# Performance work log

Measured on AMD Instinct MI355X. Metric: run time of the kernel, lower is better.

Reference implementation:

```python
import jax, jax.numpy as jnp
import numpy as np

OUT_RANGE = 6.0
OUT_SHIFT = -3.0


def setup_inputs() -> dict:
    key = jax.random.key(0)
    ks = jax.random.split(key, 6)
    B, T = 128, 64
    A, V, X = 48, 48, 96
    PF = 128
    fdim = (A + 1) * (V + 1) * (X + 1)  # 232897
    return {
        "audio_h": jax.random.normal(ks[0], (B, T, A), jnp.float32),
        "video_h": jax.random.normal(ks[1], (B, T, V), jnp.float32),
        "text_h": jax.random.normal(ks[2], (B, T, X), jnp.float32),
        "W1": jax.random.normal(ks[3], (fdim, PF), jnp.float32) * 0.002,
        "b1": jnp.zeros((PF,), jnp.float32),
        "W2": jax.random.normal(ks[4], (PF, PF), jnp.float32) * 0.05,
        "b2": jnp.zeros((PF,), jnp.float32),
        "W3": jax.random.normal(ks[5], (PF, 1), jnp.float32) * 0.05,
        "b3": jnp.zeros((1,), jnp.float32),
    }


def reference(audio_h, video_h, text_h, W1, b1, W2, b2, W3, b3):
    B, T, A = audio_h.shape
    V = video_h.shape[-1]
    X = text_h.shape[-1]
    one = jnp.ones((B, T, 1), audio_h.dtype)
    a = jnp.concatenate([one, audio_h], axis=-1)  # [B,T,A+1]
    v = jnp.concatenate([one, video_h], axis=-1)  # [B,T,V+1]
    x = jnp.concatenate([one, text_h], axis=-1)   # [B,T,X+1]
    # per-timestep triple outer product, summed over t.
    # flatten order matches torch: audio slowest, then video, text fastest.
    av = jnp.einsum("bta,btv->btav", a, v).reshape(B, T, (A + 1) * (V + 1))
    fusion = jnp.einsum("btp,btx->bpx", av, x).reshape(B, -1)  # [B,(A+1)(V+1)(X+1)]
    # dropout is identity in eval mode
    h1 = jax.nn.relu(fusion @ W1 + b1)
    h2 = jax.nn.relu(h1 @ W2 + b2)
    out = jax.nn.sigmoid(h2 @ W3 + b3) * OUT_RANGE + OUT_SHIFT  # [B,1] in (-3,3)
    return out
```

## Files before the change

kernel.cpp:

```cpp
#include <hip/hip_runtime.h>


#define B_    128
#define T_    64
#define X1    97
#define IJ    2401
#define KTOT  232897
#define PF    128
#define NGRP  19
#define PSTEPS 7376
#define KC    512
#define NB2   461

typedef short s8v __attribute__((ext_vector_type(8)));
typedef float f4v __attribute__((ext_vector_type(4)));
typedef unsigned short u8sv __attribute__((ext_vector_type(8), aligned(16)));

__device__ __forceinline__ unsigned short f2bf(float f) {
    union { float f; unsigned u; } v; v.f = f;
    return (unsigned short)((v.u + 0x7FFFu + ((v.u >> 16) & 1u)) >> 16);
}

__global__ __launch_bounds__(512) void k1_fusion(
    const float* __restrict__ audio, const float* __restrict__ video,
    const float* __restrict__ text, unsigned short* __restrict__ fusionT)
{
    __shared__ float aT[49 * 68];
    __shared__ float vT[49 * 68];
    __shared__ unsigned short xT[112 * 72];
    __shared__ __align__(16) unsigned short out_s[128 * 97];

    const int b = blockIdx.y;
    const int g = blockIdx.x;
    const int tid = threadIdx.x;

    for (int idx = tid; idx < 768; idx += 512) {
        int t = idx / 12, c = idx - t * 12;
        float4 av = *(const float4*)&audio[(b * 64 + t) * 48 + c * 4];
        float4 vv = *(const float4*)&video[(b * 64 + t) * 48 + c * 4];
        aT[(1 + c * 4 + 0) * 68 + t] = av.x; aT[(1 + c * 4 + 1) * 68 + t] = av.y;
        aT[(1 + c * 4 + 2) * 68 + t] = av.z; aT[(1 + c * 4 + 3) * 68 + t] = av.w;
        vT[(1 + c * 4 + 0) * 68 + t] = vv.x; vT[(1 + c * 4 + 1) * 68 + t] = vv.y;
        vT[(1 + c * 4 + 2) * 68 + t] = vv.z; vT[(1 + c * 4 + 3) * 68 + t] = vv.w;
    }
    for (int idx = tid; idx < 1536; idx += 512) {
        int t = idx / 24, c = idx - t * 24;
        float4 xv = *(const float4*)&text[(b * 64 + t) * 96 + c * 4];
        xT[(1 + c * 4 + 0) * 72 + t] = f2bf(xv.x);
        xT[(1 + c * 4 + 1) * 72 + t] = f2bf(xv.y);
        xT[(1 + c * 4 + 2) * 72 + t] = f2bf(xv.z);
        xT[(1 + c * 4 + 3) * 72 + t] = f2bf(xv.w);
    }
    if (tid < 64) {
        aT[tid] = 1.0f; vT[tid] = 1.0f; xT[tid] = 0x3F80;
        for (int k = 97; k < 112; ++k) xT[k * 72 + tid] = 0;
    }
    __syncthreads();

    const int wave = tid >> 6, lane = tid & 63;
    const int q = lane >> 4, ln = lane & 15;

    {
        const int ij0 = g * 128 + wave * 16;
        const int ij = ij0 + ln;
        const bool valid = ij < IJ;
        const int ijc = valid ? ij : IJ - 1;
        const int i = ijc / 49, j2 = ijc - i * 49;
        const float* ar = &aT[i * 68 + q * 8];
        const float* vr = &vT[j2 * 68 + q * 8];

        s8v af0, af1;
        #pragma unroll
        for (int j = 0; j < 8; ++j) {
            float w0 = ar[j] * vr[j];
            float w1 = ar[32 + j] * vr[32 + j];
            ((unsigned short*)&af0)[j] = valid ? f2bf(w0) : (unsigned short)0;
            ((unsigned short*)&af1)[j] = valid ? f2bf(w1) : (unsigned short)0;
        }
        #pragma unroll
        for (int nt = 0; nt < 7; ++nt) {
            s8v bf0 = *(const s8v*)&xT[(nt * 16 + ln) * 72 + q * 8];
            s8v bf1 = *(const s8v*)&xT[(nt * 16 + ln) * 72 + 32 + q * 8];
            f4v acc = {0.f, 0.f, 0.f, 0.f};
            acc = __builtin_amdgcn_mfma_f32_16x16x32_bf16(af0, bf0, acc, 0, 0, 0);
            acc = __builtin_amdgcn_mfma_f32_16x16x32_bf16(af1, bf1, acc, 0, 0, 0);
            int kk = nt * 16 + ln;
            if (kk < X1) {
                #pragma unroll
                for (int r = 0; r < 4; ++r)
                    out_s[(wave * 16 + q * 4 + r) * 97 + kk] = f2bf(acc[r]);
            }
        }
    }
    __syncthreads();

    const size_t gbase = (size_t)(g * 388) * (128 * 32) + (size_t)b * 32;
    for (int s = tid; s < 1552; s += 512) {
        u8sv v = *(const u8sv*)&out_s[s * 8];
        *(u8sv*)&fusionT[gbase + (size_t)(s >> 2) * 4096 + (s & 3) * 8] = v;
    }
}

template<bool GUARD>
__device__ __forceinline__ void k2_body(
    const unsigned short* __restrict__ fusionT, const float* __restrict__ W1,
    float* __restrict__ partials, int blk)
{
    const int tid = threadIdx.x;
    const int wave = tid >> 6, lane = tid & 63;
    const int q = lane >> 4, ln = lane & 15;
    const int f = wave * 16 + ln;
    const int kbase = blk * KC;

    const unsigned short* aptr = fusionT + (size_t)(blk * 16) * 4096 + ln * 32 + q * 8;

    f4v acc[8];
    #pragma unroll
    for (int m = 0; m < 8; ++m) acc[m] = (f4v){0.f, 0.f, 0.f, 0.f};

    s8v a_cur[8], a_nxt[8];
    float bw_cur[8], bw_nxt[8];

    #pragma unroll
    for (int j = 0; j < 8; ++j) {
        int p = kbase + q * 8 + j;
        if (GUARD) bw_cur[j] = (p < KTOT) ? W1[(size_t)p * PF + f] : 0.f;
        else       bw_cur[j] = __builtin_nontemporal_load(&W1[(size_t)p * PF + f]);
    }
    #pragma unroll
    for (int m = 0; m < 8; ++m)
        a_cur[m] = *(const s8v*)(aptr + m * 512);

    #pragma unroll
    for (int s = 0; s < 16; ++s) {
        if (s < 15) {
            const int p0 = kbase + (s + 1) * 32 + q * 8;
            #pragma unroll
            for (int j = 0; j < 8; ++j) {
                if (GUARD) bw_nxt[j] = (p0 + j < KTOT) ? W1[(size_t)(p0 + j) * PF + f] : 0.f;
                else       bw_nxt[j] = __builtin_nontemporal_load(&W1[(size_t)(p0 + j) * PF + f]);
            }
            #pragma unroll
            for (int m = 0; m < 8; ++m)
                a_nxt[m] = *(const s8v*)(aptr + (s + 1) * 4096 + m * 512);
        }
        s8v bf;
        #pragma unroll
        for (int j = 0; j < 8; ++j)
            ((unsigned short*)&bf)[j] = f2bf(bw_cur[j]);
        #pragma unroll
        for (int m = 0; m < 8; ++m)
            acc[m] = __builtin_amdgcn_mfma_f32_16x16x32_bf16(a_cur[m], bf, acc[m], 0, 0, 0);
        #pragma unroll
        for (int m = 0; m < 8; ++m) a_cur[m] = a_nxt[m];
        #pragma unroll
        for (int j = 0; j < 8; ++j) bw_cur[j] = bw_nxt[j];
    }

    float* outp = partials + (size_t)blk * 16384;
    #pragma unroll
    for (int m = 0; m < 8; ++m)
        #pragma unroll
        for (int r = 0; r < 4; ++r)
            outp[(m * 16 + q * 4 + r) * 128 + f] = acc[m][r];
}

__global__ __launch_bounds__(512, 4) void k2_gemm(
    const unsigned short* __restrict__ fusionT, const float* __restrict__ W1,
    float* __restrict__ partials)
{
    const int blk = blockIdx.x;
    if (blk >= 454) k2_body<true>(fusionT, W1, partials, blk);
    else            k2_body<false>(fusionT, W1, partials, blk);
}

__global__ __launch_bounds__(256) void k3_reduce(
    const float* __restrict__ partials, const float* __restrict__ b1,
    float* __restrict__ h1)
{
    __shared__ float red[256];
    const int e = blockIdx.x * 32 + (threadIdx.x & 31);
    const int rh = threadIdx.x >> 5;
    float s0 = 0.f, s1 = 0.f;
    int r = rh;
    for (; r + 8 < NB2; r += 16) {
        s0 += partials[(size_t)r * 16384 + e];
        s1 += partials[(size_t)(r + 8) * 16384 + e];
    }
    for (; r < NB2; r += 8) s0 += partials[(size_t)r * 16384 + e];
    red[threadIdx.x] = s0 + s1;
    __syncthreads();
    if (threadIdx.x < 32) {
        float v = 0.f;
        #pragma unroll
        for (int g = 0; g < 8; ++g) v += red[g * 32 + threadIdx.x];
        v += b1[e & 127];
        h1[e] = fmaxf(v, 0.f);
    }
}

__global__ __launch_bounds__(128) void k45_tail(
    const float* __restrict__ h1, const float* __restrict__ W2,
    const float* __restrict__ b2, const float* __restrict__ W3,
    const float* __restrict__ b3, float* __restrict__ out)
{
    __shared__ float hrow[128];
    __shared__ float h2s[128];
    const int b = blockIdx.x, f = threadIdx.x;
    hrow[f] = h1[b * 128 + f];
    __syncthreads();
    float s = b2[f];
    #pragma unroll 8
    for (int c = 0; c < 128; ++c) s += hrow[c] * W2[c * 128 + f];
    h2s[f] = fmaxf(s, 0.f) * W3[f];
    __syncthreads();
    if (f < 64) {
        float v = h2s[f] + h2s[f + 64];
        #pragma unroll
        for (int off = 32; off > 0; off >>= 1)
            v += __shfl_down(v, off, 64);
        if (f == 0) out[b] = 6.0f / (1.0f + expf(-(v + b3[0]))) - 3.0f;
    }
}

extern "C" void kernel_launch(void* const* d_in, const int* in_sizes, int n_in,
                              void* d_out, int out_size, void* d_ws, size_t ws_size,
                              hipStream_t stream)
{
    const float* audio = (const float*)d_in[0];
    const float* video = (const float*)d_in[1];
    const float* text  = (const float*)d_in[2];
    const float* W1 = (const float*)d_in[3];
    const float* b1 = (const float*)d_in[4];
    const float* W2 = (const float*)d_in[5];
    const float* b2 = (const float*)d_in[6];
    const float* W3 = (const float*)d_in[7];
    const float* b3 = (const float*)d_in[8];
    float* out = (float*)d_out;

    char* ws = (char*)d_ws;
    unsigned short* fusionT = (unsigned short*)ws;
    float* partials = (float*)(ws + 60424192);
    float* h1 = (float*)(ws + 90636288);

    k1_fusion<<<dim3(NGRP, 128), 512, 0, stream>>>(audio, video, text, fusionT);
    k2_gemm<<<dim3(NB2), 512, 0, stream>>>(fusionT, W1, partials);
    k3_reduce<<<dim3(512), 256, 0, stream>>>(partials, b1, h1);
    k45_tail<<<dim3(128), 128, 0, stream>>>(h1, W2, b2, W3, b3, out);
}
```

Before: 277.8 us.

## Halve GEMM K-chunk and fuse partial reduction with MLP tail

```diff
diff --git a/kernel.cpp b/kernel.cpp
--- a/kernel.cpp
+++ b/kernel.cpp
@@ -8,9 +8,8 @@
 #define KTOT  232897
 #define PF    128
 #define NGRP  19
-#define PSTEPS 7376
-#define KC    512
-#define NB2   461
+#define KC    256
+#define NB2   910
 
 typedef short s8v __attribute__((ext_vector_type(8)));
 typedef float f4v __attribute__((ext_vector_type(4)));
@@ -112,7 +111,7 @@
     const int f = wave * 16 + ln;
     const int kbase = blk * KC;
 
-    const unsigned short* aptr = fusionT + (size_t)(blk * 16) * 4096 + ln * 32 + q * 8;
+    const unsigned short* aptr = fusionT + (size_t)(blk * 8) * 4096 + ln * 32 + q * 8;
 
     f4v acc[8];
     #pragma unroll
@@ -132,8 +131,8 @@
         a_cur[m] = *(const s8v*)(aptr + m * 512);
 
     #pragma unroll
-    for (int s = 0; s < 16; ++s) {
-        if (s < 15) {
+    for (int s = 0; s < 8; ++s) {
+        if (s < 7) {
             const int p0 = kbase + (s + 1) * 32 + q * 8;
             #pragma unroll
             for (int j = 0; j < 8; ++j) {
@@ -170,56 +169,56 @@
     float* __restrict__ partials)
 {
     const int blk = blockIdx.x;
-    if (blk >= 454) k2_body<true>(fusionT, W1, partials, blk);
-    else            k2_body<false>(fusionT, W1, partials, blk);
-}
-
-__global__ __launch_bounds__(256) void k3_reduce(
+    if (blk == NB2 - 1) k2_body<true>(fusionT, W1, partials, blk);
+    else                k2_body<false>(fusionT, W1, partials, blk);
+}
+
+__global__ __launch_bounds__(512) void k345_tail(
     const float* __restrict__ partials, const float* __restrict__ b1,
-    float* __restrict__ h1)
-{
-    __shared__ float red[256];
-    const int e = blockIdx.x * 32 + (threadIdx.x & 31);
-    const int rh = threadIdx.x >> 5;
-    float s0 = 0.f, s1 = 0.f;
-    int r = rh;
-    for (; r + 8 < NB2; r += 16) {
-        s0 += partials[(size_t)r * 16384 + e];
-        s1 += partials[(size_t)(r + 8) * 16384 + e];
-    }
-    for (; r < NB2; r += 8) s0 += partials[(size_t)r * 16384 + e];
-    red[threadIdx.x] = s0 + s1;
-    __syncthreads();
-    if (threadIdx.x < 32) {
-        float v = 0.f;
-        #pragma unroll
-        for (int g = 0; g < 8; ++g) v += red[g * 32 + threadIdx.x];
-        v += b1[e & 127];
-        h1[e] = fmaxf(v, 0.f);
-    }
-}
-
-__global__ __launch_bounds__(128) void k45_tail(
-    const float* __restrict__ h1, const float* __restrict__ W2,
-    const float* __restrict__ b2, const float* __restrict__ W3,
-    const float* __restrict__ b3, float* __restrict__ out)
-{
+    const float* __restrict__ W2, const float* __restrict__ b2,
+    const float* __restrict__ W3, const float* __restrict__ b3,
+    float* __restrict__ out)
+{
+    __shared__ float red[512];
     __shared__ float hrow[128];
     __shared__ float h2s[128];
-    const int b = blockIdx.x, f = threadIdx.x;
-    hrow[f] = h1[b * 128 + f];
-    __syncthreads();
-    float s = b2[f];
+    const int b = blockIdx.x;
+    const int f = threadIdx.x & 127, h = threadIdx.x >> 7;
+    const int e = b * 128 + f;
+
+    float s0 = 0.f, s1 = 0.f;
+    for (int r = h; r < NB2; r += 8) {
+        s0 += partials[(size_t)r * 16384 + e];
+        if (r + 4 < NB2) s1 += partials[(size_t)(r + 4) * 16384 + e];
+    }
+    red[threadIdx.x] = s0 + s1;
+    __syncthreads();
+    if (threadIdx.x < 128) {
+        float v = red[threadIdx.x] + red[threadIdx.x + 128] +
+                  red[threadIdx.x + 256] + red[threadIdx.x + 384];
+        hrow[f] = fmaxf(v + b1[f], 0.f);
+    }
+    __syncthreads();
+
+    float s2 = 0.f;
     #pragma unroll 8
-    for (int c = 0; c < 128; ++c) s += hrow[c] * W2[c * 128 + f];
-    h2s[f] = fmaxf(s, 0.f) * W3[f];
-    __syncthreads();
-    if (f < 64) {
-        float v = h2s[f] + h2s[f + 64];
+    for (int c = h * 32; c < h * 32 + 32; ++c)
+        s2 += hrow[c] * W2[c * 128 + f];
+    red[threadIdx.x] = s2;
+    __syncthreads();
+    if (threadIdx.x < 128) {
+        float v = red[threadIdx.x] + red[threadIdx.x + 128] +
+                  red[threadIdx.x + 256] + red[threadIdx.x + 384];
+        h2s[f] = fmaxf(v + b2[f], 0.f) * W3[f];
+    }
+    __syncthreads();
+    if (threadIdx.x < 64) {
+        float v = h2s[threadIdx.x] + h2s[threadIdx.x + 64];
         #pragma unroll
         for (int off = 32; off > 0; off >>= 1)
             v += __shfl_down(v, off, 64);
-        if (f == 0) out[b] = 6.0f / (1.0f + expf(-(v + b3[0]))) - 3.0f;
+        if (threadIdx.x == 0)
+            out[b] = 6.0f / (1.0f + expf(-(v + b3[0]))) - 3.0f;
     }
 }
 
@@ -241,10 +240,8 @@
     char* ws = (char*)d_ws;
     unsigned short* fusionT = (unsigned short*)ws;
     float* partials = (float*)(ws + 60424192);
-    float* h1 = (float*)(ws + 90636288);
 
     k1_fusion<<<dim3(NGRP, 128), 512, 0, stream>>>(audio, video, text, fusionT);
     k2_gemm<<<dim3(NB2), 512, 0, stream>>>(fusionT, W1, partials);
-    k3_reduce<<<dim3(512), 256, 0, stream>>>(partials, b1, h1);
-    k45_tail<<<dim3(128), 128, 0, stream>>>(h1, W2, b2, W3, b3, out);
-}
+    k345_tail<<<dim3(128), 512, 0, stream>>>(partials, b1, W2, b2, W3, b3, out);
+}
```

New measurement: 304.8 us. 9.7% more time.
